# Kernel optimization log

Hardware: AMD Instinct MI355X
Metric: run time of the kernel (lower is better)

The kernel has to match this reference:

```python
import jax, jax.numpy as jnp
import numpy as np

B, K, N, M = 4, 512, 4096, 4
CHI2_95 = 7.815   # chi-square df=3, q=0.95
JITTER = 1e-6
ALPHA = 1.5       # sigma_cover_alpha
SIG_FLOOR = 1e-3
SIG_CEIL = 100.0
BETA = 0.85       # beta_parent_sigma
SHRINK = 1.0      # parent_sigma_shrink
KNN = 8           # fps_knn


def _sym(A):
    return 0.5 * (A + jnp.swapaxes(A, -1, -2))


def _chol3(S, eps=1e-6):
    # manual 3x3 Cholesky (vectorized, never fails), mirrors _safe_cholesky_3x3_manual
    s00, s11, s22 = S[..., 0, 0], S[..., 1, 1], S[..., 2, 2]
    s01, s02, s12 = S[..., 0, 1], S[..., 0, 2], S[..., 1, 2]
    l00 = jnp.sqrt(jnp.clip(s00, eps))
    l10 = s01 / jnp.clip(l00, eps)
    l20 = s02 / jnp.clip(l00, eps)
    l11 = jnp.sqrt(jnp.clip(s11 - l10 ** 2, eps))
    l21 = (s12 - l20 * l10) / jnp.clip(l11, eps)
    l22 = jnp.sqrt(jnp.clip(s22 - l20 ** 2 - l21 ** 2, eps))
    zz = jnp.zeros_like(l00)
    return jnp.stack([jnp.stack([l00, zz, zz], -1),
                      jnp.stack([l10, l11, zz], -1),
                      jnp.stack([l20, l21, l22], -1)], -2)


def _allocate_quota(pi, n_total, mask):
    # vectorized version of _allocate_quota: floor + largest-remainder
    valid = mask > 0.5
    pi = jnp.where(valid, pi, 0.0)
    pi = pi / jnp.clip(jnp.sum(pi, -1, keepdims=True), 1e-9)
    raw = pi * float(n_total)
    base = jnp.floor(raw)
    rem = (float(n_total) - jnp.sum(base, -1)).astype(jnp.int32)          # [B]
    frac = jnp.where(valid, raw - base, -1e9)
    order = jnp.argsort(-frac, axis=-1)
    rank = jnp.argsort(order, axis=-1)
    n_k = base.astype(jnp.int32) + (rank < rem[:, None]).astype(jnp.int32)
    return jnp.where(valid, n_k, 0)


def setup_inputs() -> dict:
    key = jax.random.key(0)
    k1, k2, k3, k4 = jax.random.split(key, 4)
    mu_p = jax.random.normal(k1, (B, K, 3), jnp.float32) * 5.0
    A = jax.random.normal(k2, (B, K, 3, 3), jnp.float32)
    Sig_p = 0.1 * jnp.einsum('bkij,bklj->bkil', A, A) + 0.5 * jnp.eye(3, dtype=jnp.float32)
    occ = jax.random.uniform(k3, (B, K), jnp.float32) + 0.1
    mask_parent = jnp.ones((B, K), jnp.float32)
    node_mask = jnp.ones((B, N), jnp.float32)
    z = jax.random.normal(k4, (B, N, M, 3), jnp.float32)
    return {"mu_p": mu_p, "Sig_p": Sig_p, "occ": occ,
            "mask_parent": mask_parent, "node_mask": node_mask, "z": z}


def reference(mu_p, Sig_p, occ, mask_parent, node_mask, z):
    b, k, _ = mu_p.shape
    n = node_mask.shape[1]
    m = z.shape[2]
    I3 = jnp.eye(3, dtype=mu_p.dtype)

    # --- quota allocation ---
    pi = occ * (mask_parent > 0.5).astype(occ.dtype)
    n_k = _allocate_quota(pi, n, mask_parent)                              # [B,K]

    # --- child -> parent assignment (packed layout, replaces Python loops) ---
    csum = jnp.cumsum(n_k, -1)                                             # [B,K]
    ar = jnp.arange(n)
    parent_idx = jax.vmap(lambda c: jnp.searchsorted(c, ar, side='right'))(csum)
    parent_idx = jnp.clip(parent_idx, 0, k - 1)                            # [B,N]

    # --- sample inside parent ellipsoid (rejection-lite) ---
    Sig_s = _sym(Sig_p * SHRINK) + JITTER * I3
    mu_c = jax.vmap(lambda a, i: a[i])(mu_p, parent_idx)                   # [B,N,3]
    Sig_c = jax.vmap(lambda a, i: a[i])(Sig_s, parent_idx)                 # [B,N,3,3]
    L = _chol3(Sig_c)                                                      # [B,N,3,3]
    cand = mu_c[:, :, None, :] + jnp.einsum('bnij,bnmj->bnmi', L, z)       # [B,N,M,3]
    # delta = cand - mu = L z, so maha2 = z^T z exactly (as in the torch code)
    maha2 = jnp.sum(z * z, -1)                                             # [B,N,M]
    inside = maha2 <= CHI2_95
    # keep first inside candidate; else smallest maha2
    score = jnp.where(inside, jnp.arange(m, dtype=maha2.dtype), 1e6 + maha2)
    pick = jnp.argmin(score, axis=-1)                                      # [B,N]
    mu0 = jnp.take_along_axis(cand, pick[..., None, None], axis=2)[:, :, 0, :]
    mu0 = mu0 * node_mask[..., None]                                       # [B,N,3]

    # --- spacing-based Sigma (kNN mean distance, isotropic) ---
    sq = jnp.sum(mu0 * mu0, -1)
    d2 = sq[:, :, None] + sq[:, None, :] - 2.0 * jnp.einsum('bnd,bmd->bnm', mu0, mu0)
    pair_ok = (node_mask[:, :, None] > 0.5) & (node_mask[:, None, :] > 0.5)
    eye = jnp.eye(n, dtype=bool)
    d2 = jnp.where(pair_ok & ~eye, d2, 1e9)
    neg_top, _ = jax.lax.top_k(-d2, KNN)                                   # [B,N,KNN]
    d_mean = jnp.mean(jnp.sqrt(jnp.clip(-neg_top, 0.0)), -1)               # [B,N]
    sigma = jnp.clip(ALPHA * d_mean, SIG_FLOOR, SIG_CEIL)
    Sig_spacing = (sigma ** 2)[..., None, None] * I3 + JITTER * I3         # [B,N,3,3]

    # --- parent/spacing Sigma blend ---
    Sig_pc = jax.vmap(lambda a, i: a[i])(_sym(Sig_p), parent_idx)
    Sig_pc = _sym(Sig_pc) + JITTER * I3
    Sig0 = BETA * Sig_pc + (1.0 - BETA) * Sig_spacing
    Sig0 = _sym(Sig0) + JITTER * I3
    Sig0 = Sig0 * node_mask[:, :, None, None]
    return mu0, Sig0, parent_idx
```

## Files before the change

### kernel.cpp

```cpp
#include <hip/hip_runtime.h>
#include <math.h>

#define B_ 4
#define K_ 512
#define N_ 4096
#define M_ 4

#define KTHREADS 512
#define SLOTS 8
#define SEGS 64
#define ROWS 16
#define CHUNK 1024
#define NCHUNK (N_ / CHUNK)
#define CPL (CHUNK / SEGS)

__device__ __forceinline__ void sort8(float s[8]) {
#define CE_(a,b) { float lo_=fminf(s[a],s[b]); float hi_=fmaxf(s[a],s[b]); s[a]=lo_; s[b]=hi_; }
    CE_(0,1) CE_(2,3) CE_(4,5) CE_(6,7)
    CE_(0,2) CE_(1,3) CE_(4,6) CE_(5,7)
    CE_(1,2) CE_(5,6)
    CE_(0,4) CE_(1,5) CE_(2,6) CE_(3,7)
    CE_(2,4) CE_(3,5)
    CE_(1,2) CE_(3,4) CE_(5,6)
#undef CE_
}

__device__ __forceinline__ void bmerge8(float k[8], const float s[8]) {
    float t0=fminf(k[0],s[7]), t1=fminf(k[1],s[6]), t2=fminf(k[2],s[5]), t3=fminf(k[3],s[4]);
    float t4=fminf(k[4],s[3]), t5=fminf(k[5],s[2]), t6=fminf(k[6],s[1]), t7=fminf(k[7],s[0]);
    float lo, hi;
    lo=fminf(t0,t4); hi=fmaxf(t0,t4); t0=lo; t4=hi;
    lo=fminf(t1,t5); hi=fmaxf(t1,t5); t1=lo; t5=hi;
    lo=fminf(t2,t6); hi=fmaxf(t2,t6); t2=lo; t6=hi;
    lo=fminf(t3,t7); hi=fmaxf(t3,t7); t3=lo; t7=hi;
    lo=fminf(t0,t2); hi=fmaxf(t0,t2); t0=lo; t2=hi;
    lo=fminf(t1,t3); hi=fmaxf(t1,t3); t1=lo; t3=hi;
    lo=fminf(t4,t6); hi=fmaxf(t4,t6); t4=lo; t6=hi;
    lo=fminf(t5,t7); hi=fmaxf(t5,t7); t5=lo; t7=hi;
    k[0]=fminf(t0,t1); k[1]=fmaxf(t0,t1);
    k[2]=fminf(t2,t3); k[3]=fmaxf(t2,t3);
    k[4]=fminf(t4,t5); k[5]=fmaxf(t4,t5);
    k[6]=fminf(t6,t7); k[7]=fmaxf(t6,t7);
}

__device__ __forceinline__ void wave_merge8(float k[8]) {
    #pragma unroll
    for (int off = 8; off <= 32; off <<= 1) {
        float bb[8];
        #pragma unroll
        for (int i = 0; i < 8; ++i) bb[i] = __shfl_xor(k[i], off, 64);
        bmerge8(k, bb);
    }
}

__global__ __launch_bounds__(512) void fused_kernel(const float* __restrict__ mu_p,
                                                    const float* __restrict__ Sig_p,
                                                    const float* __restrict__ occ,
                                                    const float* __restrict__ mask_parent,
                                                    const float* __restrict__ node_mask,
                                                    const float* __restrict__ z,
                                                    float* __restrict__ out,
                                                    float4* __restrict__ mu4,
                                                    int useF4)
{
    __shared__ double sh_a[K_];
    __shared__ double sh_part[32];
    __shared__ double sh_frac[K_];
    __shared__ int    sh_csum[K_];
    __shared__ float  csf[K_];
    __shared__ double Lsh[K_][6];
    __shared__ double s_S;
    __shared__ int    s_rem;

    int b  = blockIdx.x >> 3;
    int rb = blockIdx.x & 7;
    int k  = threadIdx.x;

    float mk = mask_parent[b * K_ + k];
    bool valid = mk > 0.5f;
    double pi = valid ? (double)occ[b * K_ + k] : 0.0;
    sh_a[k] = pi;
    __syncthreads();

    if (k < 32) {
        const double* a = sh_a + (k >> 3) * 128;
        int j = k & 7;
        double r = a[j];
        for (int i = 8; i < 128; i += 8) r += a[j + i];
        sh_part[k] = r;
    }
    __syncthreads();
    if (k == 0) {
        double pw[4];
        #pragma unroll
        for (int blk = 0; blk < 4; ++blk) {
            const double* p = sh_part + blk * 8;
            pw[blk] = ((p[0]+p[1])+(p[2]+p[3]))+((p[4]+p[5])+(p[6]+p[7]));
        }
        s_S = fmax((pw[0]+pw[1])+(pw[2]+pw[3]), 1e-9);
    }
    __syncthreads();

    double raw  = (pi / s_S) * 4096.0;
    double base = floor(raw);
    double frac = valid ? (raw - base) : -1e9;
    sh_frac[k] = frac;
    __syncthreads();
    sh_a[k] = base;
    __syncthreads();
    if (k < 32) {
        const double* a = sh_a + (k >> 3) * 128;
        int j = k & 7;
        double r = a[j];
        for (int i = 8; i < 128; i += 8) r += a[j + i];
        sh_part[k] = r;
    }
    __syncthreads();
    if (k == 0) {
        double pw[4];
        #pragma unroll
        for (int blk = 0; blk < 4; ++blk) {
            const double* p = sh_part + blk * 8;
            pw[blk] = ((p[0]+p[1])+(p[2]+p[3]))+((p[4]+p[5])+(p[6]+p[7]));
        }
        s_rem = (int)(4096.0 - ((pw[0]+pw[1])+(pw[2]+pw[3])));
    }
    __syncthreads();

    {
        double f = frac;
        int rank = 0;
        for (int j = 0; j < K_; ++j) {
            double fj = sh_frac[j];
            rank += ((fj > f) || (fj == f && j < k)) ? 1 : 0;
        }
        int nk = (int)base + (rank < s_rem ? 1 : 0);
        sh_csum[k] = valid ? nk : 0;
    }
    __syncthreads();

    for (int off = 1; off < K_; off <<= 1) {
        int v = sh_csum[k];
        int addv = (k >= off) ? sh_csum[k - off] : 0;
        __syncthreads();
        sh_csum[k] = v + addv;
        __syncthreads();
    }
    csf[k] = (float)sh_csum[k];

    {
        const float* S = Sig_p + (size_t)(b * K_ + k) * 9;
        double s00 = (double)S[0] + 1e-6;
        double s01 = 0.5 * ((double)S[1] + (double)S[3]);
        double s02 = 0.5 * ((double)S[2] + (double)S[6]);
        double s11 = (double)S[4] + 1e-6;
        double s12 = 0.5 * ((double)S[5] + (double)S[7]);
        double s22 = (double)S[8] + 1e-6;

        const double eps = 1e-6;
        double l00 = sqrt(fmax(s00, eps));
        double l10 = s01 / fmax(l00, eps);
        double l20 = s02 / fmax(l00, eps);
        double l11 = sqrt(fmax(s11 - l10 * l10, eps));
        double l21 = (s12 - l20 * l10) / fmax(l11, eps);
        double l22 = sqrt(fmax(s22 - l20 * l20 - l21 * l21, eps));

        Lsh[k][0] = l00; Lsh[k][1] = l10; Lsh[k][2] = l20;
        Lsh[k][3] = l11; Lsh[k][4] = l21; Lsh[k][5] = l22;
    }
    __syncthreads();

    int n = rb * 512 + k;
    float nf = (float)n;
    int lo = 0, hi = K_;
    while (lo < hi) {
        int mid = (lo + hi) >> 1;
        if (csf[mid] <= nf) lo = mid + 1; else hi = mid;
    }
    int p = lo < (K_ - 1) ? lo : (K_ - 1);

    double l00 = Lsh[p][0], l10 = Lsh[p][1], l20 = Lsh[p][2];
    double l11 = Lsh[p][3], l21 = Lsh[p][4], l22 = Lsh[p][5];

    const float* zp = z + (size_t)(b * N_ + n) * (M_ * 3);
    double bestScore = 1e30;
    int pick = 0;
    #pragma unroll
    for (int m = 0; m < M_; ++m) {
        double z0 = (double)zp[m*3+0], z1 = (double)zp[m*3+1], z2 = (double)zp[m*3+2];
        double maha2 = (z0 * z0 + z1 * z1) + z2 * z2;
        double score = (maha2 <= 7.815) ? (double)m : (1e6 + maha2);
        if (score < bestScore) { bestScore = score; pick = m; }
    }

    double z0 = (double)zp[pick*3+0], z1 = (double)zp[pick*3+1], z2 = (double)zp[pick*3+2];
    const float* mu = mu_p + (size_t)(b * K_ + p) * 3;
    double nm = (double)node_mask[b * N_ + n];
    double c0 = ((double)mu[0] + ((l00 * z0)))                       * nm;
    double c1 = ((double)mu[1] + ((l10 * z0 + l11 * z1)))            * nm;
    double c2 = ((double)mu[2] + ((l20 * z0 + l21 * z1) + l22 * z2)) * nm;

    size_t o = (size_t)(b * N_ + n) * 3;
    float f0 = (float)c0, f1 = (float)c1, f2 = (float)c2;
    out[o + 0] = f0;
    out[o + 1] = f1;
    out[o + 2] = f2;
    if (useF4) {
        float sq = (f0 * f0 + f1 * f1) + f2 * f2;
        mu4[b * N_ + n] = make_float4(f0, f1, f2, sq);
    }
    out[(size_t)B_ * N_ * 12 + (size_t)(b * N_ + n)] = (float)p;
}

template<bool SELF>
__device__ __forceinline__ void do_chunk(const float4* chk, int seg, int colbase,
                                         int n0, int n1,
                                         float a00, float a01, float a02,
                                         float a10, float a11, float a12,
                                         float k0[8], float k1[8])
{
    #pragma unroll
    for (int g = 0; g < CPL / 8; ++g) {
        float s0[8], s1[8];
        #pragma unroll
        for (int u = 0; u < 8; ++u) {
            int j = (g * 8 + u) * SEGS + seg;
            float4 q = chk[j];
            float d0 = fmaf(a00, q.x, fmaf(a01, q.y, fmaf(a02, q.z, q.w)));
            float d1 = fmaf(a10, q.x, fmaf(a11, q.y, fmaf(a12, q.z, q.w)));
            if (SELF) {
                int col = colbase + j;
                d0 = (col == n0) ? 3.0e38f : d0;
                d1 = (col == n1) ? 3.0e38f : d1;
            }
            s0[u] = d0;
            s1[u] = d1;
        }
        sort8(s0); bmerge8(k0, s0);
        sort8(s1); bmerge8(k1, s1);
    }
}

__global__ __launch_bounds__(KTHREADS, 4) void knn_kernel(const float* __restrict__ Sig_p,
                                                          const float* __restrict__ node_mask,
                                                          const float4* __restrict__ mu4,
                                                          int useF4,
                                                          float* __restrict__ out)
{
    __shared__ float4 chk[CHUNK];
    __shared__ float  shk[ROWS][8 * 8 + 1];

    int b   = blockIdx.x / (N_ / ROWS);
    int rb  = blockIdx.x % (N_ / ROWS);
    int tid = threadIdx.x;
    int slot = tid & (SLOTS - 1);
    int seg  = tid >> 3;

    const float* mu0 = out;
    int n0 = rb * ROWS + slot;
    int n1 = n0 + SLOTS;

    float x0, y0, z0v, x1, y1, z1v;
    if (useF4) {
        float4 p0 = mu4[b * N_ + n0]; x0 = p0.x; y0 = p0.y; z0v = p0.z;
        float4 p1 = mu4[b * N_ + n1]; x1 = p1.x; y1 = p1.y; z1v = p1.z;
    } else {
        size_t so0 = (size_t)(b * N_ + n0) * 3;
        size_t so1 = (size_t)(b * N_ + n1) * 3;
        x0 = mu0[so0]; y0 = mu0[so0+1]; z0v = mu0[so0+2];
        x1 = mu0[so1]; y1 = mu0[so1+1]; z1v = mu0[so1+2];
    }
    float a00 = -2.0f*x0, a01 = -2.0f*y0, a02 = -2.0f*z0v;
    float a10 = -2.0f*x1, a11 = -2.0f*y1, a12 = -2.0f*z1v;

    float k0[8], k1[8];
    #pragma unroll
    for (int i = 0; i < 8; ++i) { k0[i] = 3.0e38f; k1[i] = 3.0e38f; }

    int selfc = (rb * ROWS) >> 10;

    for (int c = 0; c < NCHUNK; ++c) {
        __syncthreads();
        if (useF4) {
            for (int j = tid; j < CHUNK; j += KTHREADS)
                chk[j] = mu4[b * N_ + c * CHUNK + j];
        } else {
            for (int j = tid; j < CHUNK; j += KTHREADS) {
                size_t o = (size_t)(b * N_ + c * CHUNK + j) * 3;
                float xx = mu0[o], yy = mu0[o+1], zz = mu0[o+2];
                chk[j] = make_float4(xx, yy, zz, (xx*xx + yy*yy) + zz*zz);
            }
        }
        __syncthreads();

        int colbase = c * CHUNK;
        if (c == selfc)
            do_chunk<true >(chk, seg, colbase, n0, n1, a00,a01,a02, a10,a11,a12, k0, k1);
        else
            do_chunk<false>(chk, seg, colbase, n0, n1, a00,a01,a02, a10,a11,a12, k0, k1);
    }

    wave_merge8(k0);
    wave_merge8(k1);

    int lane = tid & 63;
    int w    = tid >> 6;
    if (lane < SLOTS) {
        #pragma unroll
        for (int i = 0; i < 8; ++i) {
            shk[lane][w * 8 + i]         = k0[i];
            shk[lane + SLOTS][w * 8 + i] = k1[i];
        }
    }
    __syncthreads();

    if (tid < ROWS) {
        int r = tid;
        int nn = rb * ROWS + r;
        float best[8];
        #pragma unroll
        for (int i = 0; i < 8; ++i) best[i] = 3.0e38f;
        #pragma unroll
        for (int w2 = 0; w2 < 8; ++w2) {
            float s[8];
            #pragma unroll
            for (int i = 0; i < 8; ++i) s[i] = shk[r][w2 * 8 + i];
            bmerge8(best, s);
        }

        float cn;
        if (useF4) {
            cn = mu4[b * N_ + nn].w;
        } else {
            size_t so = (size_t)(b * N_ + nn) * 3;
            float xx = mu0[so], yy = mu0[so+1], zz = mu0[so+2];
            cn = (xx*xx + yy*yy) + zz*zz;
        }

        double s0 = sqrt(fmax((double)(cn + best[0]), 0.0)), s1 = sqrt(fmax((double)(cn + best[1]), 0.0));
        double s2 = sqrt(fmax((double)(cn + best[2]), 0.0)), s3 = sqrt(fmax((double)(cn + best[3]), 0.0));
        double s4 = sqrt(fmax((double)(cn + best[4]), 0.0)), s5 = sqrt(fmax((double)(cn + best[5]), 0.0));
        double s6 = sqrt(fmax((double)(cn + best[6]), 0.0)), s7 = sqrt(fmax((double)(cn + best[7]), 0.0));
        double d_mean = (((s0 + s1) + (s2 + s3)) + ((s4 + s5) + (s6 + s7))) / 8.0;

        double sigma = fmin(fmax(1.5 * d_mean, 1e-3), 100.0);
        double spacing = sigma * sigma + 1e-6;

        int p = (int)out[(size_t)B_ * N_ * 12 + (size_t)(b * N_ + nn)];
        const float* S = Sig_p + (size_t)(b * K_ + p) * 9;
        double s00 = (double)S[0];
        double s01 = 0.5 * ((double)S[1] + (double)S[3]);
        double s02 = 0.5 * ((double)S[2] + (double)S[6]);
        double s11 = (double)S[4];
        double s12 = 0.5 * ((double)S[5] + (double)S[7]);
        double s22 = (double)S[8];

        const double BETA = 0.85;
        const double OMB  = 1.0 - 0.85;
        double nm = (double)node_mask[b * N_ + nn];

        double d00 = (BETA * (s00 + 1e-6) + OMB * spacing) + 1e-6;
        double d11 = (BETA * (s11 + 1e-6) + OMB * spacing) + 1e-6;
        double d22 = (BETA * (s22 + 1e-6) + OMB * spacing) + 1e-6;
        double o01 = BETA * s01;
        double o02 = BETA * s02;
        double o12 = BETA * s12;

        float* Sg = out + (size_t)B_ * N_ * 3 + (size_t)(b * N_ + nn) * 9;
        Sg[0] = (float)(d00 * nm); Sg[1] = (float)(o01 * nm); Sg[2] = (float)(o02 * nm);
        Sg[3] = (float)(o01 * nm); Sg[4] = (float)(d11 * nm); Sg[5] = (float)(o12 * nm);
        Sg[6] = (float)(o02 * nm); Sg[7] = (float)(o12 * nm); Sg[8] = (float)(d22 * nm);
    }
}

extern "C" void kernel_launch(void* const* d_in, const int* in_sizes, int n_in,
                              void* d_out, int out_size, void* d_ws, size_t ws_size,
                              hipStream_t stream)
{
    const float* mu_p        = (const float*)d_in[0];
    const float* Sig_p       = (const float*)d_in[1];
    const float* occ         = (const float*)d_in[2];
    const float* mask_parent = (const float*)d_in[3];
    const float* node_mask   = (const float*)d_in[4];
    const float* z           = (const float*)d_in[5];
    float* out = (float*)d_out;

    int useF4 = (ws_size >= (size_t)B_ * N_ * sizeof(float4)) ? 1 : 0;
    float4* mu4 = (float4*)d_ws;

    fused_kernel<<<B_ * 8, 512, 0, stream>>>(mu_p, Sig_p, occ, mask_parent,
                                             node_mask, z, out, mu4, useF4);
    knn_kernel<<<B_ * (N_ / ROWS), KTHREADS, 0, stream>>>(Sig_p, node_mask,
                                                          mu4, useF4, out);
}
```

Measured before the change: 57.10 us.

## Process four rows per thread in kNN and speed up quota rank and scan

The kNN kernel now gives each thread four query rows instead of two, so every float4 candidate loaded from shared memory is reused across more rows, and the grid shrinks to half as many blocks. In the fused kernel, the O(K) rank computation runs on float copies read as float4, falling back to the exact double path only when ties occur. The shared-memory Hillis-Steele prefix sum is replaced by a wave shuffle scan plus per-wave offsets. The cost is more registers per thread in the kNN loop, which may lower occupancy, and fewer blocks to spread across the GPU.

```diff
diff --git a/kernel.cpp b/kernel.cpp
--- a/kernel.cpp
+++ b/kernel.cpp
@@ -9,7 +9,8 @@
 #define KTHREADS 512
 #define SLOTS 8
 #define SEGS 64
-#define ROWS 16
+#define RPT 4
+#define ROWSB (SLOTS * RPT)
 #define CHUNK 1024
 #define NCHUNK (N_ / CHUNK)
 #define CPL (CHUNK / SEGS)
@@ -65,10 +66,11 @@
 {
     __shared__ double sh_a[K_];
     __shared__ double sh_part[32];
-    __shared__ double sh_frac[K_];
-    __shared__ int    sh_csum[K_];
+    __shared__ alignas(16) double sh_frac[K_];
+    __shared__ alignas(16) float  sh_ffr[K_];
     __shared__ float  csf[K_];
     __shared__ double Lsh[K_][6];
+    __shared__ int    sh_wsum[8];
     __shared__ double s_S;
     __shared__ int    s_rem;
 
@@ -105,6 +107,7 @@
     double base = floor(raw);
     double frac = valid ? (raw - base) : -1e9;
     sh_frac[k] = frac;
+    sh_ffr[k]  = (float)frac;
     __syncthreads();
     sh_a[k] = base;
     __syncthreads();
@@ -127,26 +130,46 @@
     }
     __syncthreads();
 
+    int nkv = 0;
+    if (valid) {
+        float fl = (float)frac;
+        int rank = 0, eq = 0;
+        const float4* f4 = reinterpret_cast<const float4*>(sh_ffr);
+        #pragma unroll 4
+        for (int j4 = 0; j4 < K_ / 4; ++j4) {
+            float4 q = f4[j4];
+            rank += (q.x > fl) ? 1 : 0;  eq += (q.x == fl) ? 1 : 0;
+            rank += (q.y > fl) ? 1 : 0;  eq += (q.y == fl) ? 1 : 0;
+            rank += (q.z > fl) ? 1 : 0;  eq += (q.z == fl) ? 1 : 0;
+            rank += (q.w > fl) ? 1 : 0;  eq += (q.w == fl) ? 1 : 0;
+        }
+        if (__builtin_expect(eq != 1, 0)) {
+            double f = frac;
+            rank = 0;
+            for (int j = 0; j < K_; ++j) {
+                double fj = sh_frac[j];
+                rank += ((fj > f) || (fj == f && j < k)) ? 1 : 0;
+            }
+        }
+        nkv = (int)base + (rank < s_rem ? 1 : 0);
+    }
+
     {
-        double f = frac;
-        int rank = 0;
-        for (int j = 0; j < K_; ++j) {
-            double fj = sh_frac[j];
-            rank += ((fj > f) || (fj == f && j < k)) ? 1 : 0;
-        }
-        int nk = (int)base + (rank < s_rem ? 1 : 0);
-        sh_csum[k] = valid ? nk : 0;
-    }
-    __syncthreads();
-
-    for (int off = 1; off < K_; off <<= 1) {
-        int v = sh_csum[k];
-        int addv = (k >= off) ? sh_csum[k - off] : 0;
+        int lane = k & 63;
+        int w    = k >> 6;
+        int v = nkv;
+        #pragma unroll
+        for (int off = 1; off < 64; off <<= 1) {
+            int t = __shfl_up(v, off, 64);
+            v += (lane >= off) ? t : 0;
+        }
+        if (lane == 63) sh_wsum[w] = v;
         __syncthreads();
-        sh_csum[k] = v + addv;
-        __syncthreads();
-    }
-    csf[k] = (float)sh_csum[k];
+        int woff = 0;
+        #pragma unroll
+        for (int i = 0; i < 7; ++i) woff += (i < w) ? sh_wsum[i] : 0;
+        csf[k] = (float)(v + woff);
+    }
 
     {
         const float* S = Sig_p + (size_t)(b * K_ + k) * 9;
@@ -213,31 +236,28 @@
 }
 
 template<bool SELF>
-__device__ __forceinline__ void do_chunk(const float4* chk, int seg, int colbase,
-                                         int n0, int n1,
-                                         float a00, float a01, float a02,
-                                         float a10, float a11, float a12,
-                                         float k0[8], float k1[8])
+__device__ __forceinline__ void do_chunk4(const float4* chk, int seg, int colbase,
+                                          const int (&nrow)[RPT],
+                                          const float (&a)[RPT][3],
+                                          float (&kk)[RPT][8])
 {
     #pragma unroll
     for (int g = 0; g < CPL / 8; ++g) {
-        float s0[8], s1[8];
+        float s[RPT][8];
         #pragma unroll
         for (int u = 0; u < 8; ++u) {
             int j = (g * 8 + u) * SEGS + seg;
             float4 q = chk[j];
-            float d0 = fmaf(a00, q.x, fmaf(a01, q.y, fmaf(a02, q.z, q.w)));
-            float d1 = fmaf(a10, q.x, fmaf(a11, q.y, fmaf(a12, q.z, q.w)));
-            if (SELF) {
-                int col = colbase + j;
-                d0 = (col == n0) ? 3.0e38f : d0;
-                d1 = (col == n1) ? 3.0e38f : d1;
+            int col = colbase + j;
+            #pragma unroll
+            for (int r = 0; r < RPT; ++r) {
+                float d = fmaf(a[r][0], q.x, fmaf(a[r][1], q.y, fmaf(a[r][2], q.z, q.w)));
+                if (SELF) d = (col == nrow[r]) ? 3.0e38f : d;
+                s[r][u] = d;
             }
-            s0[u] = d0;
-            s1[u] = d1;
-        }
-        sort8(s0); bmerge8(k0, s0);
-        sort8(s1); bmerge8(k1, s1);
+        }
+        #pragma unroll
+        for (int r = 0; r < RPT; ++r) { sort8(s[r]); bmerge8(kk[r], s[r]); }
     }
 }
 
@@ -248,36 +268,36 @@
                                                           float* __restrict__ out)
 {
     __shared__ float4 chk[CHUNK];
-    __shared__ float  shk[ROWS][8 * 8 + 1];
-
-    int b   = blockIdx.x / (N_ / ROWS);
-    int rb  = blockIdx.x % (N_ / ROWS);
+    __shared__ float  shk[ROWSB][8 * 8 + 1];
+
+    int b   = blockIdx.x / (N_ / ROWSB);
+    int rb  = blockIdx.x % (N_ / ROWSB);
     int tid = threadIdx.x;
     int slot = tid & (SLOTS - 1);
     int seg  = tid >> 3;
 
     const float* mu0 = out;
-    int n0 = rb * ROWS + slot;
-    int n1 = n0 + SLOTS;
-
-    float x0, y0, z0v, x1, y1, z1v;
-    if (useF4) {
-        float4 p0 = mu4[b * N_ + n0]; x0 = p0.x; y0 = p0.y; z0v = p0.z;
-        float4 p1 = mu4[b * N_ + n1]; x1 = p1.x; y1 = p1.y; z1v = p1.z;
-    } else {
-        size_t so0 = (size_t)(b * N_ + n0) * 3;
-        size_t so1 = (size_t)(b * N_ + n1) * 3;
-        x0 = mu0[so0]; y0 = mu0[so0+1]; z0v = mu0[so0+2];
-        x1 = mu0[so1]; y1 = mu0[so1+1]; z1v = mu0[so1+2];
-    }
-    float a00 = -2.0f*x0, a01 = -2.0f*y0, a02 = -2.0f*z0v;
-    float a10 = -2.0f*x1, a11 = -2.0f*y1, a12 = -2.0f*z1v;
-
-    float k0[8], k1[8];
+
+    int   nrow[RPT];
+    float a[RPT][3];
+    float kk[RPT][8];
     #pragma unroll
-    for (int i = 0; i < 8; ++i) { k0[i] = 3.0e38f; k1[i] = 3.0e38f; }
-
-    int selfc = (rb * ROWS) >> 10;
+    for (int r = 0; r < RPT; ++r) {
+        int nn = rb * ROWSB + slot + r * SLOTS;
+        nrow[r] = nn;
+        float x, y, zv;
+        if (useF4) {
+            float4 p = mu4[b * N_ + nn]; x = p.x; y = p.y; zv = p.z;
+        } else {
+            size_t so = (size_t)(b * N_ + nn) * 3;
+            x = mu0[so]; y = mu0[so+1]; zv = mu0[so+2];
+        }
+        a[r][0] = -2.0f * x; a[r][1] = -2.0f * y; a[r][2] = -2.0f * zv;
+        #pragma unroll
+        for (int i = 0; i < 8; ++i) kk[r][i] = 3.0e38f;
+    }
+
+    int selfc = (rb * ROWSB) >> 10;
 
     for (int c = 0; c < NCHUNK; ++c) {
         __syncthreads();
@@ -295,28 +315,28 @@
 
         int colbase = c * CHUNK;
         if (c == selfc)
-            do_chunk<true >(chk, seg, colbase, n0, n1, a00,a01,a02, a10,a11,a12, k0, k1);
+            do_chunk4<true >(chk, seg, colbase, nrow, a, kk);
         else
-            do_chunk<false>(chk, seg, colbase, n0, n1, a00,a01,a02, a10,a11,a12, k0, k1);
-    }
-
-    wave_merge8(k0);
-    wave_merge8(k1);
+            do_chunk4<false>(chk, seg, colbase, nrow, a, kk);
+    }
+
+    #pragma unroll
+    for (int r = 0; r < RPT; ++r) wave_merge8(kk[r]);
 
     int lane = tid & 63;
     int w    = tid >> 6;
     if (lane < SLOTS) {
         #pragma unroll
-        for (int i = 0; i < 8; ++i) {
-            shk[lane][w * 8 + i]         = k0[i];
-            shk[lane + SLOTS][w * 8 + i] = k1[i];
-        }
-    }
-    __syncthreads();
-
-    if (tid < ROWS) {
+        for (int r = 0; r < RPT; ++r)
+            #pragma unroll
+            for (int i = 0; i < 8; ++i)
+                shk[lane + r * SLOTS][w * 8 + i] = kk[r][i];
+    }
+    __syncthreads();
+
+    if (tid < ROWSB) {
         int r = tid;
-        int nn = rb * ROWS + r;
+        int nn = rb * ROWSB + r;
         float best[8];
         #pragma unroll
         for (int i = 0; i < 8; ++i) best[i] = 3.0e38f;
@@ -390,6 +410,6 @@
 
     fused_kernel<<<B_ * 8, 512, 0, stream>>>(mu_p, Sig_p, occ, mask_parent,
                                              node_mask, z, out, mu4, useF4);
-    knn_kernel<<<B_ * (N_ / ROWS), KTHREADS, 0, stream>>>(Sig_p, node_mask,
-                                                          mu4, useF4, out);
-}
+    knn_kernel<<<B_ * (N_ / ROWSB), KTHREADS, 0, stream>>>(Sig_p, node_mask,
+                                                           mu4, useF4, out);
+}
```

After: 51.48 us. 1.11x faster.

## Replace rank loop with float4 fast path and prefix scan with wave shuffles

Applied to the files above, without the earlier changes.

The quota rank computation now counts greater and equal fractions using float comparisons over a float4-vectorised shared array, and falls back to the exact double tie-break loop only when ties exist. The block-wide log-step prefix sum, which used many __syncthreads, is replaced by a wave-level __shfl_up scan plus a small cross-wave offset. The kNN sort and merge helpers are rewritten as scalar-variable macros to keep the top-8 lists in registers. The float rank could disagree with the double ordering when distinct doubles round to the same float, but that case is detected through eq != 1 and sent to the exact path.

```diff
diff --git a/kernel.cpp b/kernel.cpp
--- a/kernel.cpp
+++ b/kernel.cpp
@@ -13,45 +13,31 @@
 #define CHUNK 1024
 #define NCHUNK (N_ / CHUNK)
 #define CPL (CHUNK / SEGS)
-
-__device__ __forceinline__ void sort8(float s[8]) {
-#define CE_(a,b) { float lo_=fminf(s[a],s[b]); float hi_=fmaxf(s[a],s[b]); s[a]=lo_; s[b]=hi_; }
-    CE_(0,1) CE_(2,3) CE_(4,5) CE_(6,7)
-    CE_(0,2) CE_(1,3) CE_(4,6) CE_(5,7)
-    CE_(1,2) CE_(5,6)
-    CE_(0,4) CE_(1,5) CE_(2,6) CE_(3,7)
-    CE_(2,4) CE_(3,5)
-    CE_(1,2) CE_(3,4) CE_(5,6)
-#undef CE_
-}
-
-__device__ __forceinline__ void bmerge8(float k[8], const float s[8]) {
-    float t0=fminf(k[0],s[7]), t1=fminf(k[1],s[6]), t2=fminf(k[2],s[5]), t3=fminf(k[3],s[4]);
-    float t4=fminf(k[4],s[3]), t5=fminf(k[5],s[2]), t6=fminf(k[6],s[1]), t7=fminf(k[7],s[0]);
-    float lo, hi;
-    lo=fminf(t0,t4); hi=fmaxf(t0,t4); t0=lo; t4=hi;
-    lo=fminf(t1,t5); hi=fmaxf(t1,t5); t1=lo; t5=hi;
-    lo=fminf(t2,t6); hi=fmaxf(t2,t6); t2=lo; t6=hi;
-    lo=fminf(t3,t7); hi=fmaxf(t3,t7); t3=lo; t7=hi;
-    lo=fminf(t0,t2); hi=fmaxf(t0,t2); t0=lo; t2=hi;
-    lo=fminf(t1,t3); hi=fmaxf(t1,t3); t1=lo; t3=hi;
-    lo=fminf(t4,t6); hi=fmaxf(t4,t6); t4=lo; t6=hi;
-    lo=fminf(t5,t7); hi=fmaxf(t5,t7); t5=lo; t7=hi;
-    k[0]=fminf(t0,t1); k[1]=fmaxf(t0,t1);
-    k[2]=fminf(t2,t3); k[3]=fmaxf(t2,t3);
-    k[4]=fminf(t4,t5); k[5]=fmaxf(t4,t5);
-    k[6]=fminf(t6,t7); k[7]=fmaxf(t6,t7);
-}
-
-__device__ __forceinline__ void wave_merge8(float k[8]) {
-    #pragma unroll
-    for (int off = 8; off <= 32; off <<= 1) {
-        float bb[8];
-        #pragma unroll
-        for (int i = 0; i < 8; ++i) bb[i] = __shfl_xor(k[i], off, 64);
-        bmerge8(k, bb);
-    }
-}
+#define BIGF 3.0e38f
+
+#define CSW(x,y) { float _lo = fminf(x,y); y = fmaxf(x,y); x = _lo; }
+
+#define SORT8S(s0,s1,s2,s3,s4,s5,s6,s7) \
+    CSW(s0,s1) CSW(s2,s3) CSW(s4,s5) CSW(s6,s7) \
+    CSW(s0,s2) CSW(s1,s3) CSW(s4,s6) CSW(s5,s7) \
+    CSW(s1,s2) CSW(s5,s6) \
+    CSW(s0,s4) CSW(s1,s5) CSW(s2,s6) CSW(s3,s7) \
+    CSW(s2,s4) CSW(s3,s5) \
+    CSW(s1,s2) CSW(s3,s4) CSW(s5,s6)
+
+#define BMERGE8S(K0,K1,K2,K3,K4,K5,K6,K7, S0,S1,S2,S3,S4,S5,S6,S7) \
+    K0 = fminf(K0,S7); K1 = fminf(K1,S6); K2 = fminf(K2,S5); K3 = fminf(K3,S4); \
+    K4 = fminf(K4,S3); K5 = fminf(K5,S2); K6 = fminf(K6,S1); K7 = fminf(K7,S0); \
+    CSW(K0,K4) CSW(K1,K5) CSW(K2,K6) CSW(K3,K7) \
+    CSW(K0,K2) CSW(K1,K3) CSW(K4,K6) CSW(K5,K7) \
+    CSW(K0,K1) CSW(K2,K3) CSW(K4,K5) CSW(K6,K7)
+
+#define WMERGE(K0,K1,K2,K3,K4,K5,K6,K7, off) { \
+    float _b0 = __shfl_xor(K0, off, 64); float _b1 = __shfl_xor(K1, off, 64); \
+    float _b2 = __shfl_xor(K2, off, 64); float _b3 = __shfl_xor(K3, off, 64); \
+    float _b4 = __shfl_xor(K4, off, 64); float _b5 = __shfl_xor(K5, off, 64); \
+    float _b6 = __shfl_xor(K6, off, 64); float _b7 = __shfl_xor(K7, off, 64); \
+    BMERGE8S(K0,K1,K2,K3,K4,K5,K6,K7, _b0,_b1,_b2,_b3,_b4,_b5,_b6,_b7) }
 
 __global__ __launch_bounds__(512) void fused_kernel(const float* __restrict__ mu_p,
                                                     const float* __restrict__ Sig_p,
@@ -65,10 +51,11 @@
 {
     __shared__ double sh_a[K_];
     __shared__ double sh_part[32];
-    __shared__ double sh_frac[K_];
-    __shared__ int    sh_csum[K_];
+    __shared__ alignas(16) double sh_frac[K_];
+    __shared__ alignas(16) float  sh_ffr[K_];
     __shared__ float  csf[K_];
     __shared__ double Lsh[K_][6];
+    __shared__ int    sh_wsum[8];
     __shared__ double s_S;
     __shared__ int    s_rem;
 
@@ -105,6 +92,7 @@
     double base = floor(raw);
     double frac = valid ? (raw - base) : -1e9;
     sh_frac[k] = frac;
+    sh_ffr[k]  = (float)frac;
     __syncthreads();
     sh_a[k] = base;
     __syncthreads();
@@ -127,26 +115,46 @@
     }
     __syncthreads();
 
+    int nkv = 0;
+    if (valid) {
+        float fl = (float)frac;
+        int rank = 0, eq = 0;
+        const float4* f4 = reinterpret_cast<const float4*>(sh_ffr);
+        #pragma unroll 4
+        for (int j4 = 0; j4 < K_ / 4; ++j4) {
+            float4 q = f4[j4];
+            rank += (q.x > fl) ? 1 : 0;  eq += (q.x == fl) ? 1 : 0;
+            rank += (q.y > fl) ? 1 : 0;  eq += (q.y == fl) ? 1 : 0;
+            rank += (q.z > fl) ? 1 : 0;  eq += (q.z == fl) ? 1 : 0;
+            rank += (q.w > fl) ? 1 : 0;  eq += (q.w == fl) ? 1 : 0;
+        }
+        if (__builtin_expect(eq != 1, 0)) {
+            double f = frac;
+            rank = 0;
+            for (int j = 0; j < K_; ++j) {
+                double fj = sh_frac[j];
+                rank += ((fj > f) || (fj == f && j < k)) ? 1 : 0;
+            }
+        }
+        nkv = (int)base + (rank < s_rem ? 1 : 0);
+    }
+
     {
-        double f = frac;
-        int rank = 0;
-        for (int j = 0; j < K_; ++j) {
-            double fj = sh_frac[j];
-            rank += ((fj > f) || (fj == f && j < k)) ? 1 : 0;
-        }
-        int nk = (int)base + (rank < s_rem ? 1 : 0);
-        sh_csum[k] = valid ? nk : 0;
-    }
-    __syncthreads();
-
-    for (int off = 1; off < K_; off <<= 1) {
-        int v = sh_csum[k];
-        int addv = (k >= off) ? sh_csum[k - off] : 0;
+        int lane = k & 63;
+        int w    = k >> 6;
+        int v = nkv;
+        #pragma unroll
+        for (int off = 1; off < 64; off <<= 1) {
+            int t = __shfl_up(v, off, 64);
+            v += (lane >= off) ? t : 0;
+        }
+        if (lane == 63) sh_wsum[w] = v;
         __syncthreads();
-        sh_csum[k] = v + addv;
-        __syncthreads();
-    }
-    csf[k] = (float)sh_csum[k];
+        int woff = 0;
+        #pragma unroll
+        for (int i = 0; i < 7; ++i) woff += (i < w) ? sh_wsum[i] : 0;
+        csf[k] = (float)(v + woff);
+    }
 
     {
         const float* S = Sig_p + (size_t)(b * K_ + k) * 9;
@@ -212,34 +220,23 @@
     out[(size_t)B_ * N_ * 12 + (size_t)(b * N_ + n)] = (float)p;
 }
 
-template<bool SELF>
-__device__ __forceinline__ void do_chunk(const float4* chk, int seg, int colbase,
-                                         int n0, int n1,
-                                         float a00, float a01, float a02,
-                                         float a10, float a11, float a12,
-                                         float k0[8], float k1[8])
-{
-    #pragma unroll
-    for (int g = 0; g < CPL / 8; ++g) {
-        float s0[8], s1[8];
-        #pragma unroll
-        for (int u = 0; u < 8; ++u) {
-            int j = (g * 8 + u) * SEGS + seg;
-            float4 q = chk[j];
-            float d0 = fmaf(a00, q.x, fmaf(a01, q.y, fmaf(a02, q.z, q.w)));
-            float d1 = fmaf(a10, q.x, fmaf(a11, q.y, fmaf(a12, q.z, q.w)));
-            if (SELF) {
-                int col = colbase + j;
-                d0 = (col == n0) ? 3.0e38f : d0;
-                d1 = (col == n1) ? 3.0e38f : d1;
-            }
-            s0[u] = d0;
-            s1[u] = d1;
-        }
-        sort8(s0); bmerge8(k0, s0);
-        sort8(s1); bmerge8(k1, s1);
-    }
-}
+#define LOADU(u, SQ) { \
+    int j_ = (gb8 + u) * SEGS + seg; \
+    float4 q_ = chk[j_]; \
+    s##u = fmaf(a00, q_.x, fmaf(a01, q_.y, fmaf(a02, q_.z, q_.w))); \
+    r##u = fmaf(a10, q_.x, fmaf(a11, q_.y, fmaf(a12, q_.z, q_.w))); \
+    if (SQ) { int c_ = colbase + j_; \
+        s##u = (c_ == n0) ? BIGF : s##u; \
+        r##u = (c_ == n1) ? BIGF : r##u; } }
+
+#define GROUP8(SQ) { \
+    float s0,s1,s2,s3,s4,s5,s6,s7, r0,r1,r2,r3,r4,r5,r6,r7; \
+    LOADU(0,SQ) LOADU(1,SQ) LOADU(2,SQ) LOADU(3,SQ) \
+    LOADU(4,SQ) LOADU(5,SQ) LOADU(6,SQ) LOADU(7,SQ) \
+    SORT8S(s0,s1,s2,s3,s4,s5,s6,s7) \
+    BMERGE8S(ka0,ka1,ka2,ka3,ka4,ka5,ka6,ka7, s0,s1,s2,s3,s4,s5,s6,s7) \
+    SORT8S(r0,r1,r2,r3,r4,r5,r6,r7) \
+    BMERGE8S(kb0,kb1,kb2,kb3,kb4,kb5,kb6,kb7, r0,r1,r2,r3,r4,r5,r6,r7) }
 
 __global__ __launch_bounds__(KTHREADS, 4) void knn_kernel(const float* __restrict__ Sig_p,
                                                           const float* __restrict__ node_mask,
@@ -273,9 +270,8 @@
     float a00 = -2.0f*x0, a01 = -2.0f*y0, a02 = -2.0f*z0v;
     float a10 = -2.0f*x1, a11 = -2.0f*y1, a12 = -2.0f*z1v;
 
-    float k0[8], k1[8];
-    #pragma unroll
-    for (int i = 0; i < 8; ++i) { k0[i] = 3.0e38f; k1[i] = 3.0e38f; }
+    float ka0=BIGF,ka1=BIGF,ka2=BIGF,ka3=BIGF,ka4=BIGF,ka5=BIGF,ka6=BIGF,ka7=BIGF;
+    float kb0=BIGF,kb1=BIGF,kb2=BIGF,kb3=BIGF,kb4=BIGF,kb5=BIGF,kb6=BIGF,kb7=BIGF;
 
     int selfc = (rb * ROWS) >> 10;
 
@@ -294,38 +290,47 @@
         __syncthreads();
 
         int colbase = c * CHUNK;
-        if (c == selfc)
-            do_chunk<true >(chk, seg, colbase, n0, n1, a00,a01,a02, a10,a11,a12, k0, k1);
-        else
-            do_chunk<false>(chk, seg, colbase, n0, n1, a00,a01,a02, a10,a11,a12, k0, k1);
-    }
-
-    wave_merge8(k0);
-    wave_merge8(k1);
+        if (c == selfc) {
+            { int gb8 = 0; GROUP8(1) }
+            { int gb8 = 8; GROUP8(1) }
+        } else {
+            { int gb8 = 0; GROUP8(0) }
+            { int gb8 = 8; GROUP8(0) }
+        }
+    }
+
+    WMERGE(ka0,ka1,ka2,ka3,ka4,ka5,ka6,ka7, 8)
+    WMERGE(ka0,ka1,ka2,ka3,ka4,ka5,ka6,ka7, 16)
+    WMERGE(ka0,ka1,ka2,ka3,ka4,ka5,ka6,ka7, 32)
+    WMERGE(kb0,kb1,kb2,kb3,kb4,kb5,kb6,kb7, 8)
+    WMERGE(kb0,kb1,kb2,kb3,kb4,kb5,kb6,kb7, 16)
+    WMERGE(kb0,kb1,kb2,kb3,kb4,kb5,kb6,kb7, 32)
 
     int lane = tid & 63;
     int w    = tid >> 6;
     if (lane < SLOTS) {
-        #pragma unroll
-        for (int i = 0; i < 8; ++i) {
-            shk[lane][w * 8 + i]         = k0[i];
-            shk[lane + SLOTS][w * 8 + i] = k1[i];
-        }
+        shk[lane][w*8+0] = ka0; shk[lane][w*8+1] = ka1;
+        shk[lane][w*8+2] = ka2; shk[lane][w*8+3] = ka3;
+        shk[lane][w*8+4] = ka4; shk[lane][w*8+5] = ka5;
+        shk[lane][w*8+6] = ka6; shk[lane][w*8+7] = ka7;
+        shk[lane+SLOTS][w*8+0] = kb0; shk[lane+SLOTS][w*8+1] = kb1;
+        shk[lane+SLOTS][w*8+2] = kb2; shk[lane+SLOTS][w*8+3] = kb3;
+        shk[lane+SLOTS][w*8+4] = kb4; shk[lane+SLOTS][w*8+5] = kb5;
+        shk[lane+SLOTS][w*8+6] = kb6; shk[lane+SLOTS][w*8+7] = kb7;
     }
     __syncthreads();
 
     if (tid < ROWS) {
         int r = tid;
         int nn = rb * ROWS + r;
-        float best[8];
-        #pragma unroll
-        for (int i = 0; i < 8; ++i) best[i] = 3.0e38f;
+        float e0=BIGF,e1=BIGF,e2=BIGF,e3=BIGF,e4=BIGF,e5=BIGF,e6=BIGF,e7=BIGF;
         #pragma unroll
         for (int w2 = 0; w2 < 8; ++w2) {
-            float s[8];
-            #pragma unroll
-            for (int i = 0; i < 8; ++i) s[i] = shk[r][w2 * 8 + i];
-            bmerge8(best, s);
+            float b0 = shk[r][w2*8+0], b1 = shk[r][w2*8+1];
+            float b2 = shk[r][w2*8+2], b3 = shk[r][w2*8+3];
+            float b4 = shk[r][w2*8+4], b5 = shk[r][w2*8+5];
+            float b6 = shk[r][w2*8+6], b7 = shk[r][w2*8+7];
+            BMERGE8S(e0,e1,e2,e3,e4,e5,e6,e7, b0,b1,b2,b3,b4,b5,b6,b7)
         }
 
         float cn;
@@ -337,10 +342,10 @@
             cn = (xx*xx + yy*yy) + zz*zz;
         }
 
-        double s0 = sqrt(fmax((double)(cn + best[0]), 0.0)), s1 = sqrt(fmax((double)(cn + best[1]), 0.0));
-        double s2 = sqrt(fmax((double)(cn + best[2]), 0.0)), s3 = sqrt(fmax((double)(cn + best[3]), 0.0));
-        double s4 = sqrt(fmax((double)(cn + best[4]), 0.0)), s5 = sqrt(fmax((double)(cn + best[5]), 0.0));
-        double s6 = sqrt(fmax((double)(cn + best[6]), 0.0)), s7 = sqrt(fmax((double)(cn + best[7]), 0.0));
+        double s0 = sqrt(fmax((double)(cn + e0), 0.0)), s1 = sqrt(fmax((double)(cn + e1), 0.0));
+        double s2 = sqrt(fmax((double)(cn + e2), 0.0)), s3 = sqrt(fmax((double)(cn + e3), 0.0));
+        double s4 = sqrt(fmax((double)(cn + e4), 0.0)), s5 = sqrt(fmax((double)(cn + e5), 0.0));
+        double s6 = sqrt(fmax((double)(cn + e6), 0.0)), s7 = sqrt(fmax((double)(cn + e7), 0.0));
         double d_mean = (((s0 + s1) + (s2 + s3)) + ((s4 + s5) + (s6 + s7))) / 8.0;
 
         double sigma = fmin(fmax(1.5 * d_mean, 1e-3), 100.0);
```

Result: faster. 49.74 us (-12.9%).
